# Optimization experiments

Hardware: AMD Instinct MI355X
Metric: run time of the kernel (lower is better)

The kernel has to match this reference:

```python
import jax, jax.numpy as jnp
import numpy as np

INPUT_NDIMS = 1024
HIDDEN = 512
LATENT = 50
BATCH = 16384

def setup_inputs() -> dict:
    key = jax.random.key(0)
    ks = jax.random.split(key, 12)
    s = 0.02
    x = jax.random.uniform(ks[0], (BATCH, INPUT_NDIMS), dtype=jnp.float32)
    u = 0.01 + 0.98 * jax.random.uniform(ks[1], (BATCH, LATENT), dtype=jnp.float32)
    W1 = s * jax.random.normal(ks[2], (HIDDEN, INPUT_NDIMS), dtype=jnp.float32)
    b1 = jnp.zeros((HIDDEN,), jnp.float32)
    Wa = s * jax.random.normal(ks[3], (LATENT, HIDDEN), dtype=jnp.float32)
    ba = jnp.zeros((LATENT,), jnp.float32)
    Wb = s * jax.random.normal(ks[4], (LATENT, HIDDEN), dtype=jnp.float32)
    bb = jnp.zeros((LATENT,), jnp.float32)
    W2 = s * jax.random.normal(ks[5], (HIDDEN, LATENT), dtype=jnp.float32)
    b2 = jnp.zeros((HIDDEN,), jnp.float32)
    W3 = s * jax.random.normal(ks[6], (INPUT_NDIMS, HIDDEN), dtype=jnp.float32)
    b3 = jnp.zeros((INPUT_NDIMS,), jnp.float32)
    return dict(x=x, u=u, W1=W1, b1=b1, Wa=Wa, ba=ba, Wb=Wb, bb=bb, W2=W2, b2=b2, W3=W3, b3=b3)

def _stick_segments(v):
    # pi[:, k] = v[:, k] * prod_{j<k} (1 - v[:, j])  -- single O(K) cumprod pass
    cp = jnp.cumprod(1.0 - v, axis=1)                       # inclusive cumprod
    excl = jnp.concatenate([jnp.ones_like(cp[:, :1]), cp[:, :-1]], axis=1)
    return v * excl

def reference(x, u, W1, b1, Wa, ba, Wb, bb, W2, b2, W3, b3):
    # encoder: MLP -> positive Kumaraswamy params alpha (param1), beta (param2)
    h = jax.nn.relu(x @ W1.T + b1)                           # [B, H]
    alpha = jax.nn.softplus(h @ Wa.T + ba) + 1e-4            # [B, K]
    beta = jax.nn.softplus(h @ Wb.T + bb) + 1e-4             # [B, K]
    # Kumaraswamy reparameterized sample: v = (1 - u^(1/beta))^(1/alpha)
    v = jnp.power(1.0 - jnp.power(u, 1.0 / beta), 1.0 / alpha)
    # set_v_K_to_one: force last stick fraction to 1 so segments sum to 1
    v = v.at[:, -1].set(1.0)
    pi = _stick_segments(v)                                  # [B, K], rows sum to 1
    # decoder: MLP with sigmoid output
    h2 = jax.nn.relu(pi @ W2.T + b2)                         # [B, H]
    recon = jax.nn.sigmoid(h2 @ W3.T + b3)                   # [B, D]
    return recon, alpha, beta
```

## Files before the change

### kernel.cpp

```cpp
#include <hip/hip_runtime.h>
#include <hip/hip_bf16.h>

typedef __hip_bfloat16 bf16_t;
typedef __attribute__((ext_vector_type(4))) float f32x4;
typedef __attribute__((ext_vector_type(8))) __bf16 bf16x8;
typedef __attribute__((ext_vector_type(8))) short s16x8;
typedef __attribute__((ext_vector_type(4))) unsigned short u16x4;

#define BATCH 16384
#define NDIM  1024
#define HID   512
#define LAT   50

#define LOG2E 1.44269504088896340736f
#define RLOG2E 0.69314718055994530942f

__device__ __forceinline__ float ex2(float x) { return __builtin_amdgcn_exp2f(x); }
__device__ __forceinline__ float lg2(float x) { return __builtin_amdgcn_logf(x); }
__device__ __forceinline__ float rcp(float x) { return __builtin_amdgcn_rcpf(x); }

__device__ inline unsigned short f2b_u(float f) {
  union { bf16_t b; unsigned short u; } cv; cv.b = __float2bfloat16(f); return cv.u;
}

__device__ __forceinline__ void gload16(const void* src, void* dst_lds) {
  __builtin_amdgcn_global_load_lds(
      reinterpret_cast<const __attribute__((address_space(1))) void*>(
          reinterpret_cast<unsigned long long>(src)),
      reinterpret_cast<__attribute__((address_space(3))) void*>(
          static_cast<unsigned>(reinterpret_cast<unsigned long long>(dst_lds))),
      16, 0, 0);
}

__global__ void prep_w_kernel(const float* __restrict__ W1, const float* __restrict__ W3,
                              const float* __restrict__ Wa, const float* __restrict__ Wb,
                              const float* __restrict__ W2, const float* __restrict__ ba,
                              const float* __restrict__ bb,
                              bf16_t* __restrict__ w1, bf16_t* __restrict__ w3,
                              bf16_t* __restrict__ wab, bf16_t* __restrict__ w2p,
                              float* __restrict__ bab)
{
  const int W1U  = (HID * NDIM) / 4;
  const int W3U  = (NDIM * HID) / 4;
  const int WABN = 128 * HID;
  const int W2PN = HID * 64;
  const int TOT  = W1U + W3U + WABN + W2PN + 128;
  for (int i = blockIdx.x * blockDim.x + threadIdx.x; i < TOT;
       i += gridDim.x * blockDim.x) {
    int j = i;
    if (j < W1U) {
      const f32x4 v = ((const f32x4*)W1)[j];
      u16x4 o; o[0]=f2b_u(v[0]); o[1]=f2b_u(v[1]); o[2]=f2b_u(v[2]); o[3]=f2b_u(v[3]);
      ((u16x4*)w1)[j] = o; continue;
    }
    j -= W1U;
    if (j < W3U) {
      const f32x4 v = ((const f32x4*)W3)[j];
      u16x4 o; o[0]=f2b_u(v[0]); o[1]=f2b_u(v[1]); o[2]=f2b_u(v[2]); o[3]=f2b_u(v[3]);
      ((u16x4*)w3)[j] = o; continue;
    }
    j -= W3U;
    if (j < WABN) {
      const int n = j >> 9, k = j & 511;
      float v = (n < 50) ? Wa[n * 512 + k] : ((n < 100) ? Wb[(n - 50) * 512 + k] : 0.f);
      wab[j] = __float2bfloat16(v); continue;
    }
    j -= WABN;
    if (j < W2PN) {
      const int n = j >> 6, k = j & 63;
      w2p[j] = __float2bfloat16(k < 50 ? W2[n * 50 + k] : 0.f); continue;
    }
    j -= W2PN;
    bab[j] = (j < 50) ? ba[j] : ((j < 100) ? bb[j - 50] : 0.f);
  }
}

template<int A_F32, int EPI>
__global__ __launch_bounds__(256, 2)
void gemm_kernel(const void* __restrict__ Av, const bf16_t* __restrict__ B,
                 const float* __restrict__ bias, void* __restrict__ out0,
                 float* __restrict__ out_a, float* __restrict__ out_b,
                 int M, int N, int K)
{
  __shared__ char lds[32768];
  char* lA = lds;
  char* lB = lds + 16384;

  const int tid  = threadIdx.x;
  const int mblocks = M >> 7;
  const int bm   = blockIdx.x % mblocks;
  const int bn   = blockIdx.x / mblocks;
  const int wid  = tid >> 6;
  const int lane = tid & 63;
  const int l15  = lane & 15;
  const int l4   = lane >> 4;
  const int wm   = (wid >> 1) << 6;
  const int wn   = (wid & 1) << 6;
  const int uw   = __builtin_amdgcn_readfirstlane(wid);

  f32x4 acc[4][4] = {};

  for (int k0 = 0; k0 < K; k0 += 64) {
    #pragma unroll
    for (int i = 0; i < 4; ++i) {
      const int c  = (i * 4 + uw) * 64 + lane;
      const int r  = c >> 3;
      const int sp = c & 7;
      const int sl = sp ^ (r & 7);
      gload16(B + (size_t)(bn * 128 + r) * K + k0 + sl * 8,
              lB + (i * 4 + uw) * 1024);
    }
    if (A_F32) {
      const float* A = (const float*)Av;
      #pragma unroll
      for (int i = 0; i < 4; ++i) {
        const int c  = i * 256 + tid;
        const int r  = c >> 3;
        const int sl = c & 7;
        const int sp = sl ^ (r & 7);
        const float* s = A + (size_t)(bm * 128 + r) * K + k0 + sl * 8;
        const f32x4 v0 = *(const f32x4*)s;
        const f32x4 v1 = *(const f32x4*)(s + 4);
        union { s16x8 v; unsigned short us[8]; } o;
        o.us[0]=f2b_u(v0[0]); o.us[1]=f2b_u(v0[1]); o.us[2]=f2b_u(v0[2]); o.us[3]=f2b_u(v0[3]);
        o.us[4]=f2b_u(v1[0]); o.us[5]=f2b_u(v1[1]); o.us[6]=f2b_u(v1[2]); o.us[7]=f2b_u(v1[3]);
        *(s16x8*)(lA + r * 128 + sp * 16) = o.v;
      }
    } else {
      const bf16_t* A = (const bf16_t*)Av;
      #pragma unroll
      for (int i = 0; i < 4; ++i) {
        const int c  = (i * 4 + uw) * 64 + lane;
        const int r  = c >> 3;
        const int sp = c & 7;
        const int sl = sp ^ (r & 7);
        gload16(A + (size_t)(bm * 128 + r) * K + k0 + sl * 8,
                lA + (i * 4 + uw) * 1024);
      }
    }
    __syncthreads();

    #pragma unroll
    for (int h = 0; h < 2; ++h) {
      bf16x8 af[4], bfr[4];
      #pragma unroll
      for (int mi = 0; mi < 4; ++mi) {
        const int row = wm + mi * 16 + l15;
        const int sp  = (h * 4 + l4) ^ (row & 7);
        af[mi] = *(const bf16x8*)(lA + row * 128 + sp * 16);
      }
      #pragma unroll
      for (int ni = 0; ni < 4; ++ni) {
        const int row = wn + ni * 16 + l15;
        const int sp  = (h * 4 + l4) ^ (row & 7);
        bfr[ni] = *(const bf16x8*)(lB + row * 128 + sp * 16);
      }
      #pragma unroll
      for (int mi = 0; mi < 4; ++mi)
        #pragma unroll
        for (int ni = 0; ni < 4; ++ni)
          acc[mi][ni] = __builtin_amdgcn_mfma_f32_16x16x32_bf16(
              af[mi], bfr[ni], acc[mi][ni], 0, 0, 0);
    }
    __syncthreads();
  }

  #pragma unroll
  for (int ni = 0; ni < 4; ++ni) {
    const int n  = bn * 128 + wn + ni * 16 + l15;
    const float bv = bias[n];
    #pragma unroll
    for (int mi = 0; mi < 4; ++mi) {
      #pragma unroll
      for (int r = 0; r < 4; ++r) {
        const int m  = bm * 128 + wm + mi * 16 + l4 * 4 + r;
        const float t = acc[mi][ni][r] + bv;
        if (EPI == 2) {
          if (n < 100) {
            const float y =
                (t > 20.f ? t : lg2(1.f + ex2(t * LOG2E)) * RLOG2E) + 1e-4f;
            if (n < 50) out_a[(size_t)m * 50 + n] = y;
            else        out_b[(size_t)m * 50 + (n - 50)] = y;
          }
        } else if (EPI == 0) {
          ((bf16_t*)out0)[(size_t)m * N + n] = __float2bfloat16(fmaxf(t, 0.f));
        } else {
          ((float*)out0)[(size_t)m * N + n] = rcp(1.f + ex2(-t * LOG2E));
        }
      }
    }
  }
}

__global__ void stick_kernel(const float* __restrict__ u,
                             const float* __restrict__ alpha,
                             const float* __restrict__ beta,
                             bf16_t* __restrict__ pi)
{
  const int gw   = (blockIdx.x * blockDim.x + threadIdx.x) >> 6;
  const int lane = threadIdx.x & 63;
  if (gw >= BATCH) return;
  const size_t row = (size_t)gw;

  float v = 1.f, t = 1.f;
  if (lane < 49) {
    const float a  = alpha[row * 50 + lane];
    const float b  = beta[row * 50 + lane];
    const float uu = u[row * 50 + lane];
    const float tb = ex2(lg2(uu) * rcp(b));
    v = ex2(lg2(1.f - tb) * rcp(a));
    t = 1.f - v;
  }
  float p = t;
  #pragma unroll
  for (int d = 1; d < 64; d <<= 1) {
    const float o = __shfl_up(p, d, 64);
    if (lane >= d) p *= o;
  }
  float e = __shfl_up(p, 1, 64);
  if (lane == 0) e = 1.f;
  pi[row * 64 + lane] = __float2bfloat16(lane < 50 ? v * e : 0.f);
}

extern "C" void kernel_launch(void* const* d_in, const int* in_sizes, int n_in,
                              void* d_out, int out_size, void* d_ws, size_t ws_size,
                              hipStream_t stream)
{
  const float* x  = (const float*)d_in[0];
  const float* u  = (const float*)d_in[1];
  const float* W1 = (const float*)d_in[2];
  const float* b1 = (const float*)d_in[3];
  const float* Wa = (const float*)d_in[4];
  const float* ba = (const float*)d_in[5];
  const float* Wb = (const float*)d_in[6];
  const float* bb = (const float*)d_in[7];
  const float* W2 = (const float*)d_in[8];
  const float* b2 = (const float*)d_in[9];
  const float* W3 = (const float*)d_in[10];
  const float* b3 = (const float*)d_in[11];

  float* recon  = (float*)d_out;
  float* oalpha = recon + (size_t)BATCH * NDIM;
  float* obeta  = oalpha + (size_t)BATCH * LAT;

  char* ws = (char*)d_ws;
  bf16_t* h   = (bf16_t*)(ws);
  bf16_t* h2  = (bf16_t*)(ws + 16777216);
  bf16_t* pi  = (bf16_t*)(ws + 33554432);
  bf16_t* w1  = (bf16_t*)(ws + 35651584);
  bf16_t* w3  = (bf16_t*)(ws + 36700160);
  bf16_t* wab = (bf16_t*)(ws + 37748736);
  bf16_t* w2p = (bf16_t*)(ws + 37879808);
  float*  bab = (float*)(ws + 37945344);

  prep_w_kernel<<<512, 256, 0, stream>>>(W1, W3, Wa, Wb, W2, ba, bb,
                                         w1, w3, wab, w2p, bab);
  gemm_kernel<1, 0><<<512, 256, 0, stream>>>(
      x, w1, b1, (void*)h, nullptr, nullptr, BATCH, HID, NDIM);
  gemm_kernel<0, 2><<<128, 256, 0, stream>>>(
      h, wab, bab, nullptr, oalpha, obeta, BATCH, 128, HID);
  stick_kernel<<<4096, 256, 0, stream>>>(u, oalpha, obeta, pi);
  gemm_kernel<0, 0><<<512, 256, 0, stream>>>(
      pi, w2p, b2, (void*)h2, nullptr, nullptr, BATCH, HID, 64);
  gemm_kernel<0, 1><<<1024, 256, 0, stream>>>(
      h2, w3, b3, (void*)recon, nullptr, nullptr, BATCH, NDIM, HID);
}
```

Baseline: 96.22 us.

## Load fp32 A tiles via async global-to-LDS, add M-tile template and block swizzle

The first GEMM now copies fp32 x tiles directly into LDS with async 16-byte loads and converts them to bf16 when reading fragments, instead of converting in registers before the LDS store. The GEMM gains an M-tile template parameter so the small-N GEMMs use 64-row tiles and launch twice as many blocks for better CU occupancy. Block indices are remapped with an XCD-style swizzle and N-major ordering to improve L2 reuse of A rows across chiplets. The cost is doubled LDS for the fp32 path (48KB per block) and conversion work repeated per fragment read.

```diff
diff --git a/kernel.cpp b/kernel.cpp
--- a/kernel.cpp
+++ b/kernel.cpp
@@ -75,30 +75,33 @@
   }
 }
 
-template<int A_F32, int EPI>
+template<int A_F32, int EPI, int MT>
 __global__ __launch_bounds__(256, 2)
 void gemm_kernel(const void* __restrict__ Av, const bf16_t* __restrict__ B,
                  const float* __restrict__ bias, void* __restrict__ out0,
                  float* __restrict__ out_a, float* __restrict__ out_b,
                  int M, int N, int K)
 {
-  __shared__ char lds[32768];
+  constexpr int MI   = MT / 32;
+  constexpr int LDSA = A_F32 ? 32768 : MT * 128;
+  __shared__ char lds[LDSA + 16384];
   char* lA = lds;
-  char* lB = lds + 16384;
+  char* lB = lds + LDSA;
 
   const int tid  = threadIdx.x;
-  const int mblocks = M >> 7;
-  const int bm   = blockIdx.x % mblocks;
-  const int bn   = blockIdx.x / mblocks;
+  const int swzid = ((blockIdx.x & 7) * (gridDim.x >> 3)) + (blockIdx.x >> 3);
+  const int nblocks = N >> 7;
+  const int bn   = swzid % nblocks;
+  const int bm   = swzid / nblocks;
   const int wid  = tid >> 6;
   const int lane = tid & 63;
   const int l15  = lane & 15;
   const int l4   = lane >> 4;
-  const int wm   = (wid >> 1) << 6;
+  const int wm   = (wid >> 1) * (MT / 2);
   const int wn   = (wid & 1) << 6;
   const int uw   = __builtin_amdgcn_readfirstlane(wid);
 
-  f32x4 acc[4][4] = {};
+  f32x4 acc[MI][4] = {};
 
   for (int k0 = 0; k0 < K; k0 += 64) {
     #pragma unroll
@@ -113,28 +116,23 @@
     if (A_F32) {
       const float* A = (const float*)Av;
       #pragma unroll
-      for (int i = 0; i < 4; ++i) {
-        const int c  = i * 256 + tid;
-        const int r  = c >> 3;
-        const int sl = c & 7;
-        const int sp = sl ^ (r & 7);
-        const float* s = A + (size_t)(bm * 128 + r) * K + k0 + sl * 8;
-        const f32x4 v0 = *(const f32x4*)s;
-        const f32x4 v1 = *(const f32x4*)(s + 4);
-        union { s16x8 v; unsigned short us[8]; } o;
-        o.us[0]=f2b_u(v0[0]); o.us[1]=f2b_u(v0[1]); o.us[2]=f2b_u(v0[2]); o.us[3]=f2b_u(v0[3]);
-        o.us[4]=f2b_u(v1[0]); o.us[5]=f2b_u(v1[1]); o.us[6]=f2b_u(v1[2]); o.us[7]=f2b_u(v1[3]);
-        *(s16x8*)(lA + r * 128 + sp * 16) = o.v;
+      for (int i = 0; i < 8; ++i) {
+        const int c  = (i * 4 + uw) * 64 + lane;
+        const int r  = c >> 4;
+        const int sp = c & 15;
+        const int sl = sp ^ (r & 15);
+        gload16(A + (size_t)(bm * MT + r) * K + k0 + sl * 4,
+                lA + (i * 4 + uw) * 1024);
       }
     } else {
       const bf16_t* A = (const bf16_t*)Av;
       #pragma unroll
-      for (int i = 0; i < 4; ++i) {
+      for (int i = 0; i < MI; ++i) {
         const int c  = (i * 4 + uw) * 64 + lane;
         const int r  = c >> 3;
         const int sp = c & 7;
         const int sl = sp ^ (r & 7);
-        gload16(A + (size_t)(bm * 128 + r) * K + k0 + sl * 8,
+        gload16(A + (size_t)(bm * MT + r) * K + k0 + sl * 8,
                 lA + (i * 4 + uw) * 1024);
       }
     }
@@ -142,12 +140,22 @@
 
     #pragma unroll
     for (int h = 0; h < 2; ++h) {
-      bf16x8 af[4], bfr[4];
-      #pragma unroll
-      for (int mi = 0; mi < 4; ++mi) {
+      bf16x8 af[MI], bfr[4];
+      #pragma unroll
+      for (int mi = 0; mi < MI; ++mi) {
         const int row = wm + mi * 16 + l15;
-        const int sp  = (h * 4 + l4) ^ (row & 7);
-        af[mi] = *(const bf16x8*)(lA + row * 128 + sp * 16);
+        if (A_F32) {
+          const int sl0 = (h * 4 + l4) * 2;
+          const f32x4 v0 = *(const f32x4*)(lA + row * 256 + (sl0 ^ (row & 15)) * 16);
+          const f32x4 v1 = *(const f32x4*)(lA + row * 256 + ((sl0 + 1) ^ (row & 15)) * 16);
+          union { bf16x8 v; unsigned short us[8]; } o;
+          o.us[0]=f2b_u(v0[0]); o.us[1]=f2b_u(v0[1]); o.us[2]=f2b_u(v0[2]); o.us[3]=f2b_u(v0[3]);
+          o.us[4]=f2b_u(v1[0]); o.us[5]=f2b_u(v1[1]); o.us[6]=f2b_u(v1[2]); o.us[7]=f2b_u(v1[3]);
+          af[mi] = o.v;
+        } else {
+          const int sp = (h * 4 + l4) ^ (row & 7);
+          af[mi] = *(const bf16x8*)(lA + row * 128 + sp * 16);
+        }
       }
       #pragma unroll
       for (int ni = 0; ni < 4; ++ni) {
@@ -156,7 +164,7 @@
         bfr[ni] = *(const bf16x8*)(lB + row * 128 + sp * 16);
       }
       #pragma unroll
-      for (int mi = 0; mi < 4; ++mi)
+      for (int mi = 0; mi < MI; ++mi)
         #pragma unroll
         for (int ni = 0; ni < 4; ++ni)
           acc[mi][ni] = __builtin_amdgcn_mfma_f32_16x16x32_bf16(
@@ -170,10 +178,10 @@
     const int n  = bn * 128 + wn + ni * 16 + l15;
     const float bv = bias[n];
     #pragma unroll
-    for (int mi = 0; mi < 4; ++mi) {
+    for (int mi = 0; mi < MI; ++mi) {
       #pragma unroll
       for (int r = 0; r < 4; ++r) {
-        const int m  = bm * 128 + wm + mi * 16 + l4 * 4 + r;
+        const int m  = bm * MT + wm + mi * 16 + l4 * 4 + r;
         const float t = acc[mi][ni][r] + bv;
         if (EPI == 2) {
           if (n < 100) {
@@ -255,13 +263,13 @@
 
   prep_w_kernel<<<512, 256, 0, stream>>>(W1, W3, Wa, Wb, W2, ba, bb,
                                          w1, w3, wab, w2p, bab);
-  gemm_kernel<1, 0><<<512, 256, 0, stream>>>(
+  gemm_kernel<1, 0, 128><<<512, 256, 0, stream>>>(
       x, w1, b1, (void*)h, nullptr, nullptr, BATCH, HID, NDIM);
-  gemm_kernel<0, 2><<<128, 256, 0, stream>>>(
+  gemm_kernel<0, 2, 64><<<256, 256, 0, stream>>>(
       h, wab, bab, nullptr, oalpha, obeta, BATCH, 128, HID);
   stick_kernel<<<4096, 256, 0, stream>>>(u, oalpha, obeta, pi);
-  gemm_kernel<0, 0><<<512, 256, 0, stream>>>(
+  gemm_kernel<0, 0, 64><<<1024, 256, 0, stream>>>(
       pi, w2p, b2, (void*)h2, nullptr, nullptr, BATCH, HID, 64);
-  gemm_kernel<0, 1><<<1024, 256, 0, stream>>>(
+  gemm_kernel<0, 1, 128><<<1024, 256, 0, stream>>>(
       h2, w3, b3, (void*)recon, nullptr, nullptr, BATCH, NDIM, HID);
 }
```

Result: faster. 85.40 us (-11.2%).
